# Kernel optimization log

Measured on AMD Instinct MI355X. Metric: run time of the kernel, lower is better.

The kernel has to match this reference:

```python
import jax, jax.numpy as jnp
import numpy as np

DIM = 2048
NUM_LADDERS = 3
DEPTH = 5
EPS = 0.01


def setup_inputs() -> dict:
    key = jax.random.key(0)
    ks = jax.random.split(key, 5)
    s = 1.0 / np.sqrt(DIM)
    x = jax.random.normal(ks[0], (4, 2048, DIM), dtype=jnp.float32)
    U_w = jax.random.uniform(ks[1], (DIM, DIM), jnp.float32, -s, s)          # U.weight  [out,in]
    gate_w = jax.random.uniform(ks[2], (DIM, DIM), jnp.float32, -s, s)       # gate_proj.weight
    ladder_w = jax.random.uniform(ks[3], (NUM_LADDERS, DEPTH + 1, DIM), jnp.float32, -s, s)
    V_w = jax.random.uniform(ks[4], (DIM, NUM_LADDERS), jnp.float32, -1.0 / np.sqrt(NUM_LADDERS), 1.0 / np.sqrt(NUM_LADDERS))
    return {"x": x, "U_w": U_w, "gate_w": gate_w, "ladder_w": ladder_w, "V_w": V_w}


def _continued_fraction(a_cf, eps):
    # a_cf: (..., depth). Evaluate a_1/(1 + a_2/(1 + ... a_d/1)) with
    # epsilon-guarded denominators (pole avoidance).
    d = a_cf.shape[-1]
    f = jnp.zeros(a_cf.shape[:-1], a_cf.dtype)
    for k in reversed(range(d)):  # tiny fixed depth: loop is fine
        denom = 1.0 + f
        denom = jnp.where(jnp.abs(denom) < eps,
                          jnp.where(denom >= 0, eps, -eps), denom)
        f = a_cf[..., k] / denom
    return f


def reference(x, U_w, gate_w, ladder_w, V_w):
    linear_out = jnp.einsum('bsd,od->bso', x, U_w)                 # U(x)
    gated_x = jax.nn.sigmoid(jnp.einsum('bsd,od->bso', x, gate_w)) * x
    # All ladders at once: (b,s,L,depth+1)
    a = jnp.einsum('bsd,lkd->bslk', gated_x, ladder_w)
    a0 = a[..., 0]                                                 # (b,s,L)
    z = a0 + _continued_fraction(a[..., 1:], EPS)                  # (b,s,L)
    combined = jnp.einsum('bsl,dl->bsd', z, V_w)                   # V(z)
    return linear_out + combined
```

## Files before the change

### kernel.cpp

```cpp
#include <hip/hip_runtime.h>
#include <cstdint>
#include <cstddef>

#define DIM 2048
#define NROWS 8192
#define NL 3
#define DEPTH 5
#define CF_EPS 0.01f

typedef __attribute__((ext_vector_type(8))) __bf16 bfrag;
typedef __attribute__((ext_vector_type(4))) float f32x4;

typedef __attribute__((address_space(1))) void gvoid;
typedef __attribute__((address_space(3))) void lvoid;

__device__ __forceinline__ void gld_lds16(const void* g, void* l) {
    __builtin_amdgcn_global_load_lds((gvoid*)g, (lvoid*)l, 16, 0, 0);
}

template<bool SPLIT>
__global__ __launch_bounds__(256) void mfma_gemm(
    const ushort* __restrict__ Ah, const ushort* __restrict__ Al,
    const ushort* __restrict__ Bh, const ushort* __restrict__ Bl,
    float* __restrict__ C)
{
    constexpr int BK = 32;
    __shared__ __align__(16) ushort sAh[128 * BK];
    __shared__ __align__(16) ushort sBh[128 * BK];
    __shared__ __align__(16) ushort sAl[SPLIT ? 128 * BK : 8];
    __shared__ __align__(16) ushort sBl[SPLIT ? 128 * BK : 8];

    const int tid  = threadIdx.x;
    const int wave = tid >> 6;
    const int lane = tid & 63;
    const int wm   = wave & 1;
    const int wn   = wave >> 1;
    const int m0   = blockIdx.y * 128;
    const int n0   = blockIdx.x * 128;

    const size_t soff = (size_t)(wave * 32 + (lane >> 2)) * DIM + (lane & 3) * 8;
    const ushort* gA  = Ah + (size_t)m0 * DIM + soff;
    const ushort* gB  = Bh + (size_t)n0 * DIM + soff;
    const ushort* gAl = Al + (size_t)m0 * DIM + soff;
    const ushort* gBl = Bl + (size_t)n0 * DIM + soff;

    ushort* lA0 = &sAh[(wave * 32) * BK];
    ushort* lA1 = &sAh[(wave * 32 + 16) * BK];
    ushort* lB0 = &sBh[(wave * 32) * BK];
    ushort* lB1 = &sBh[(wave * 32 + 16) * BK];
    ushort* lAl0 = &sAl[SPLIT ? (wave * 32) * BK : 0];
    ushort* lAl1 = &sAl[SPLIT ? (wave * 32 + 16) * BK : 0];
    ushort* lBl0 = &sBl[SPLIT ? (wave * 32) * BK : 0];
    ushort* lBl1 = &sBl[SPLIT ? (wave * 32 + 16) * BK : 0];

    const int fm = lane & 15;
    const int fq = lane >> 4;

    f32x4 acc[4][4];
    #pragma unroll
    for (int i = 0; i < 4; ++i)
        #pragma unroll
        for (int j = 0; j < 4; ++j)
            acc[i][j] = (f32x4){0.f, 0.f, 0.f, 0.f};

    for (int k0 = 0; k0 < DIM; k0 += BK) {
        __syncthreads();
        gld_lds16(gA + k0, lA0);
        gld_lds16(gA + (size_t)16 * DIM + k0, lA1);
        gld_lds16(gB + k0, lB0);
        gld_lds16(gB + (size_t)16 * DIM + k0, lB1);
        if constexpr (SPLIT) {
            gld_lds16(gAl + k0, lAl0);
            gld_lds16(gAl + (size_t)16 * DIM + k0, lAl1);
            gld_lds16(gBl + k0, lBl0);
            gld_lds16(gBl + (size_t)16 * DIM + k0, lBl1);
        }
        __syncthreads();

        bfrag ah[4], bh[4], al[4], bl[4];
        #pragma unroll
        for (int i = 0; i < 4; ++i) {
            ah[i] = *(const bfrag*)&sAh[(wm * 64 + i * 16 + fm) * BK + fq * 8];
            bh[i] = *(const bfrag*)&sBh[(wn * 64 + i * 16 + fm) * BK + fq * 8];
            if constexpr (SPLIT) {
                al[i] = *(const bfrag*)&sAl[(wm * 64 + i * 16 + fm) * BK + fq * 8];
                bl[i] = *(const bfrag*)&sBl[(wn * 64 + i * 16 + fm) * BK + fq * 8];
            }
        }
        #pragma unroll
        for (int i = 0; i < 4; ++i)
            #pragma unroll
            for (int j = 0; j < 4; ++j) {
                acc[i][j] = __builtin_amdgcn_mfma_f32_16x16x32_bf16(ah[i], bh[j], acc[i][j], 0, 0, 0);
                if constexpr (SPLIT) {
                    acc[i][j] = __builtin_amdgcn_mfma_f32_16x16x32_bf16(ah[i], bl[j], acc[i][j], 0, 0, 0);
                    acc[i][j] = __builtin_amdgcn_mfma_f32_16x16x32_bf16(al[i], bh[j], acc[i][j], 0, 0, 0);
                }
            }
    }

    #pragma unroll
    for (int i = 0; i < 4; ++i) {
        const int rowb = m0 + wm * 64 + i * 16 + fq * 4;
        #pragma unroll
        for (int j = 0; j < 4; ++j) {
            const int col = n0 + wn * 64 + j * 16 + fm;
            #pragma unroll
            for (int r = 0; r < 4; ++r)
                C[(size_t)(rowb + r) * DIM + col] = acc[i][j][r];
        }
    }
}

__device__ __forceinline__ ushort f2bf_bits(float f) {
    __bf16 h = (__bf16)f;
    return __builtin_bit_cast(unsigned short, h);
}
__device__ __forceinline__ float bfbits2f(ushort u) {
    __bf16 h = __builtin_bit_cast(__bf16, u);
    return (float)h;
}

union U16x8 { ushort u[8]; uint4 v; };

__global__ __launch_bounds__(256) void split2(const float* __restrict__ src,
                                              ushort* __restrict__ hi,
                                              ushort* __restrict__ lo)
{
    const size_t i0 = ((size_t)blockIdx.x * 256 + threadIdx.x) * 8;
    const float4 v0 = *(const float4*)(src + i0);
    const float4 v1 = *(const float4*)(src + i0 + 4);
    const float f[8] = {v0.x, v0.y, v0.z, v0.w, v1.x, v1.y, v1.z, v1.w};
    U16x8 h, l;
    #pragma unroll
    for (int j = 0; j < 8; ++j) {
        const ushort hb = f2bf_bits(f[j]);
        h.u[j] = hb;
        l.u[j] = f2bf_bits(f[j] - bfbits2f(hb));
    }
    *(uint4*)(hi + i0) = h.v;
    *(uint4*)(lo + i0) = l.v;
}

__global__ __launch_bounds__(256) void tobf16(const float* __restrict__ src,
                                              ushort* __restrict__ dst)
{
    const size_t i0 = ((size_t)blockIdx.x * 256 + threadIdx.x) * 8;
    const float4 v0 = *(const float4*)(src + i0);
    const float4 v1 = *(const float4*)(src + i0 + 4);
    const float f[8] = {v0.x, v0.y, v0.z, v0.w, v1.x, v1.y, v1.z, v1.w};
    U16x8 h;
    #pragma unroll
    for (int j = 0; j < 8; ++j) h.u[j] = f2bf_bits(f[j]);
    *(uint4*)(dst + i0) = h.v;
}

#define BMF 128
#define BNF 128
#define BKF 16
#define LDAF 132

__global__ __launch_bounds__(256) void sgemm_dual(
    const float* __restrict__ X,
    const float* __restrict__ Uw,
    const float* __restrict__ Gw,
    float* __restrict__ outLin,
    float* __restrict__ outGate)
{
    __shared__ float As[BKF][LDAF];
    __shared__ float Bs[BKF][LDAF];

    const int tid = threadIdx.x;
    const int n0 = blockIdx.x * BNF;
    const int m0 = blockIdx.y * BMF;
    const bool isGate = (n0 >= DIM);
    const float* W = isGate ? Gw : Uw;
    float* C = isGate ? outGate : outLin;
    const int nb = isGate ? (n0 - DIM) : n0;

    const int lr = tid >> 2;
    const int lc = (tid & 3) << 2;

    const float* pa0 = X + (size_t)(m0 + lr) * DIM + lc;
    const float* pa1 = X + (size_t)(m0 + lr + 64) * DIM + lc;
    const float* pb0 = W + (size_t)(nb + lr) * DIM + lc;
    const float* pb1 = W + (size_t)(nb + lr + 64) * DIM + lc;

    const int tx = tid & 15;
    const int ty = tid >> 4;

    float acc[8][8];
    #pragma unroll
    for (int i = 0; i < 8; ++i)
        #pragma unroll
        for (int j = 0; j < 8; ++j) acc[i][j] = 0.f;

    for (int k0 = 0; k0 < DIM; k0 += BKF) {
        const float4 a0 = *(const float4*)(pa0 + k0);
        const float4 a1 = *(const float4*)(pa1 + k0);
        const float4 b0 = *(const float4*)(pb0 + k0);
        const float4 b1 = *(const float4*)(pb1 + k0);
        __syncthreads();
        As[lc + 0][lr] = a0.x; As[lc + 1][lr] = a0.y; As[lc + 2][lr] = a0.z; As[lc + 3][lr] = a0.w;
        As[lc + 0][lr + 64] = a1.x; As[lc + 1][lr + 64] = a1.y; As[lc + 2][lr + 64] = a1.z; As[lc + 3][lr + 64] = a1.w;
        Bs[lc + 0][lr] = b0.x; Bs[lc + 1][lr] = b0.y; Bs[lc + 2][lr] = b0.z; Bs[lc + 3][lr] = b0.w;
        Bs[lc + 0][lr + 64] = b1.x; Bs[lc + 1][lr + 64] = b1.y; Bs[lc + 2][lr + 64] = b1.z; Bs[lc + 3][lr + 64] = b1.w;
        __syncthreads();
        #pragma unroll
        for (int kk = 0; kk < BKF; ++kk) {
            float av[8], bv[8];
            *(float4*)&av[0] = *(const float4*)&As[kk][ty * 8];
            *(float4*)&av[4] = *(const float4*)&As[kk][ty * 8 + 4];
            *(float4*)&bv[0] = *(const float4*)&Bs[kk][tx * 8];
            *(float4*)&bv[4] = *(const float4*)&Bs[kk][tx * 8 + 4];
            #pragma unroll
            for (int i = 0; i < 8; ++i)
                #pragma unroll
                for (int j = 0; j < 8; ++j)
                    acc[i][j] = fmaf(av[i], bv[j], acc[i][j]);
        }
    }

    #pragma unroll
    for (int i = 0; i < 8; ++i) {
        float* crow = C + (size_t)(m0 + ty * 8 + i) * DIM + nb + tx * 8;
        *(float4*)crow       = make_float4(acc[i][0], acc[i][1], acc[i][2], acc[i][3]);
        *(float4*)(crow + 4) = make_float4(acc[i][4], acc[i][5], acc[i][6], acc[i][7]);
    }
}

__global__ __launch_bounds__(256) void ladder_epilogue(
    const float* __restrict__ X,
    const float* __restrict__ G,
    const float* __restrict__ Lw,
    const float* __restrict__ Vw,
    float* __restrict__ Out)
{
    const int r = blockIdx.x;
    const int tid = threadIdx.x;
    const int d0 = tid * 8;
    const float* xrow = X + (size_t)r * DIM;
    const float* grow = G + (size_t)r * DIM;

    const float4 xv0 = *(const float4*)(xrow + d0);
    const float4 xv1 = *(const float4*)(xrow + d0 + 4);
    const float4 gv0 = *(const float4*)(grow + d0);
    const float4 gv1 = *(const float4*)(grow + d0 + 4);

    float gated[8];
    {
        const float gx[8] = {gv0.x, gv0.y, gv0.z, gv0.w, gv1.x, gv1.y, gv1.z, gv1.w};
        const float xx[8] = {xv0.x, xv0.y, xv0.z, xv0.w, xv1.x, xv1.y, xv1.z, xv1.w};
        #pragma unroll
        for (int j = 0; j < 8; ++j) {
            const float s = 1.0f / (1.0f + __expf(-gx[j]));
            gated[j] = s * xx[j];
        }
    }

    float part[NL * (DEPTH + 1)];
    #pragma unroll
    for (int lk = 0; lk < NL * (DEPTH + 1); ++lk) {
        const float* lrow = Lw + (size_t)lk * DIM + d0;
        const float4 w0 = *(const float4*)lrow;
        const float4 w1 = *(const float4*)(lrow + 4);
        part[lk] = gated[0] * w0.x + gated[1] * w0.y + gated[2] * w0.z + gated[3] * w0.w
                 + gated[4] * w1.x + gated[5] * w1.y + gated[6] * w1.z + gated[7] * w1.w;
    }

    #pragma unroll
    for (int off = 32; off > 0; off >>= 1) {
        #pragma unroll
        for (int lk = 0; lk < NL * (DEPTH + 1); ++lk)
            part[lk] += __shfl_down(part[lk], off, 64);
    }

    __shared__ float red[4][NL * (DEPTH + 1)];
    __shared__ float zsh[NL];
    const int wave = tid >> 6;
    const int lane = tid & 63;
    if (lane == 0) {
        #pragma unroll
        for (int lk = 0; lk < NL * (DEPTH + 1); ++lk) red[wave][lk] = part[lk];
    }
    __syncthreads();
    if (tid < NL) {
        float a[DEPTH + 1];
        #pragma unroll
        for (int k = 0; k < DEPTH + 1; ++k)
            a[k] = red[0][tid * 6 + k] + red[1][tid * 6 + k]
                 + red[2][tid * 6 + k] + red[3][tid * 6 + k];
        float f = 0.f;
        #pragma unroll
        for (int k = DEPTH - 1; k >= 0; --k) {
            float denom = 1.f + f;
            if (fabsf(denom) < CF_EPS) denom = (denom >= 0.f) ? CF_EPS : -CF_EPS;
            f = a[k + 1] / denom;
        }
        zsh[tid] = a[0] + f;
    }
    __syncthreads();
    const float z0 = zsh[0], z1 = zsh[1], z2 = zsh[2];

    float* orow = Out + (size_t)r * DIM + d0;
    const float4 o0 = *(const float4*)orow;
    const float4 o1 = *(const float4*)(orow + 4);
    float ov[8] = {o0.x, o0.y, o0.z, o0.w, o1.x, o1.y, o1.z, o1.w};
    #pragma unroll
    for (int j = 0; j < 8; ++j) {
        const float* vp = Vw + (size_t)(d0 + j) * NL;
        ov[j] += z0 * vp[0] + z1 * vp[1] + z2 * vp[2];
    }
    *(float4*)orow       = make_float4(ov[0], ov[1], ov[2], ov[3]);
    *(float4*)(orow + 4) = make_float4(ov[4], ov[5], ov[6], ov[7]);
}

extern "C" void kernel_launch(void* const* d_in, const int* in_sizes, int n_in,
                              void* d_out, int out_size, void* d_ws, size_t ws_size,
                              hipStream_t stream) {
    const float* X  = (const float*)d_in[0];
    const float* Uw = (const float*)d_in[1];
    const float* Gw = (const float*)d_in[2];
    const float* Lw = (const float*)d_in[3];
    const float* Vw = (const float*)d_in[4];
    float* out = (float*)d_out;

    const size_t WS_NEED = 159383552ull;
    char* ws = (char*)d_ws;
    float* gbuf = (float*)ws;

    if (ws_size >= WS_NEED) {
        ushort* Xh  = (ushort*)(ws + 67108864);
        ushort* Xl  = (ushort*)(ws + 100663296);
        ushort* Gwh = (ushort*)(ws + 134217728);
        ushort* Gwl = (ushort*)(ws + 142606336);
        ushort* Uwh = (ushort*)(ws + 150994944);

        split2<<<dim3(8192), dim3(256), 0, stream>>>(X, Xh, Xl);
        split2<<<dim3(2048), dim3(256), 0, stream>>>(Gw, Gwh, Gwl);
        tobf16<<<dim3(2048), dim3(256), 0, stream>>>(Uw, Uwh);

        dim3 grid(DIM / 128, NROWS / 128);
        mfma_gemm<false><<<grid, dim3(256), 0, stream>>>(Xh, Xh, Uwh, Uwh, out);
        mfma_gemm<true ><<<grid, dim3(256), 0, stream>>>(Xh, Xl, Gwh, Gwl, gbuf);
    } else {
        dim3 grid(2 * DIM / BNF, NROWS / BMF);
        sgemm_dual<<<grid, dim3(256), 0, stream>>>(X, Uw, Gw, out, gbuf);
    }
    ladder_epilogue<<<dim3(NROWS), dim3(256), 0, stream>>>(X, gbuf, Lw, Vw, out);
}
```

Measured before the change: 577.9 us.

## Fuse ladder projection into gate GEMM epilogue and V(z) into U GEMM

```diff
diff --git a/kernel.cpp b/kernel.cpp
--- a/kernel.cpp
+++ b/kernel.cpp
@@ -6,6 +6,7 @@
 #define NROWS 8192
 #define NL 3
 #define DEPTH 5
+#define NLK 18
 #define CF_EPS 0.01f
 
 typedef __attribute__((ext_vector_type(8))) __bf16 bfrag;
@@ -18,17 +19,14 @@
     __builtin_amdgcn_global_load_lds((gvoid*)g, (lvoid*)l, 16, 0, 0);
 }
 
-template<bool SPLIT>
-__global__ __launch_bounds__(256) void mfma_gemm(
-    const ushort* __restrict__ Ah, const ushort* __restrict__ Al,
-    const ushort* __restrict__ Bh, const ushort* __restrict__ Bl,
+__global__ __launch_bounds__(256) void mfma_gemm_u(
+    const ushort* __restrict__ A, const ushort* __restrict__ B,
+    const float* __restrict__ zb, const float* __restrict__ Vp,
     float* __restrict__ C)
 {
     constexpr int BK = 32;
-    __shared__ __align__(16) ushort sAh[128 * BK];
-    __shared__ __align__(16) ushort sBh[128 * BK];
-    __shared__ __align__(16) ushort sAl[SPLIT ? 128 * BK : 8];
-    __shared__ __align__(16) ushort sBl[SPLIT ? 128 * BK : 8];
+    __shared__ __align__(16) ushort sA[128 * BK];
+    __shared__ __align__(16) ushort sB[128 * BK];
 
     const int tid  = threadIdx.x;
     const int wave = tid >> 6;
@@ -39,19 +37,13 @@
     const int n0   = blockIdx.x * 128;
 
     const size_t soff = (size_t)(wave * 32 + (lane >> 2)) * DIM + (lane & 3) * 8;
-    const ushort* gA  = Ah + (size_t)m0 * DIM + soff;
-    const ushort* gB  = Bh + (size_t)n0 * DIM + soff;
-    const ushort* gAl = Al + (size_t)m0 * DIM + soff;
-    const ushort* gBl = Bl + (size_t)n0 * DIM + soff;
-
-    ushort* lA0 = &sAh[(wave * 32) * BK];
-    ushort* lA1 = &sAh[(wave * 32 + 16) * BK];
-    ushort* lB0 = &sBh[(wave * 32) * BK];
-    ushort* lB1 = &sBh[(wave * 32 + 16) * BK];
-    ushort* lAl0 = &sAl[SPLIT ? (wave * 32) * BK : 0];
-    ushort* lAl1 = &sAl[SPLIT ? (wave * 32 + 16) * BK : 0];
-    ushort* lBl0 = &sBl[SPLIT ? (wave * 32) * BK : 0];
-    ushort* lBl1 = &sBl[SPLIT ? (wave * 32 + 16) * BK : 0];
+    const ushort* gA = A + (size_t)m0 * DIM + soff;
+    const ushort* gB = B + (size_t)n0 * DIM + soff;
+
+    ushort* lA0 = &sA[(wave * 32) * BK];
+    ushort* lA1 = &sA[(wave * 32 + 16) * BK];
+    ushort* lB0 = &sB[(wave * 32) * BK];
+    ushort* lB1 = &sB[(wave * 32 + 16) * BK];
 
     const int fm = lane & 15;
     const int fq = lane >> 4;
@@ -69,12 +61,100 @@
         gld_lds16(gA + (size_t)16 * DIM + k0, lA1);
         gld_lds16(gB + k0, lB0);
         gld_lds16(gB + (size_t)16 * DIM + k0, lB1);
-        if constexpr (SPLIT) {
-            gld_lds16(gAl + k0, lAl0);
-            gld_lds16(gAl + (size_t)16 * DIM + k0, lAl1);
-            gld_lds16(gBl + k0, lBl0);
-            gld_lds16(gBl + (size_t)16 * DIM + k0, lBl1);
-        }
+        __syncthreads();
+
+        bfrag ah[4], bh[4];
+        #pragma unroll
+        for (int i = 0; i < 4; ++i) {
+            ah[i] = *(const bfrag*)&sA[(wm * 64 + i * 16 + fm) * BK + fq * 8];
+            bh[i] = *(const bfrag*)&sB[(wn * 64 + i * 16 + fm) * BK + fq * 8];
+        }
+        #pragma unroll
+        for (int i = 0; i < 4; ++i)
+            #pragma unroll
+            for (int j = 0; j < 4; ++j)
+                acc[i][j] = __builtin_amdgcn_mfma_f32_16x16x32_bf16(ah[i], bh[j], acc[i][j], 0, 0, 0);
+    }
+
+    float4 vc[4];
+    #pragma unroll
+    for (int j = 0; j < 4; ++j)
+        vc[j] = *(const float4*)&Vp[(size_t)(n0 + wn * 64 + j * 16 + fm) * 4];
+
+    #pragma unroll
+    for (int i = 0; i < 4; ++i) {
+        const int rowb = m0 + wm * 64 + i * 16 + fq * 4;
+        #pragma unroll
+        for (int r = 0; r < 4; ++r) {
+            const float4 zr = *(const float4*)&zb[(size_t)(rowb + r) * 4];
+            #pragma unroll
+            for (int j = 0; j < 4; ++j) {
+                const int col = n0 + wn * 64 + j * 16 + fm;
+                C[(size_t)(rowb + r) * DIM + col] =
+                    acc[i][j][r] + zr.x * vc[j].x + zr.y * vc[j].y + zr.z * vc[j].z;
+            }
+        }
+    }
+}
+
+__global__ __launch_bounds__(256) void mfma_gemm_gate(
+    const ushort* __restrict__ Ah, const ushort* __restrict__ Al,
+    const ushort* __restrict__ Bh, const ushort* __restrict__ Bl,
+    const float* __restrict__ X,  const float* __restrict__ Lw,
+    float* __restrict__ a_buf)
+{
+    constexpr int BK = 32;
+    __shared__ __align__(16) char smem[32768];
+    ushort* sAh = (ushort*)(smem);
+    ushort* sBh = (ushort*)(smem + 8192);
+    ushort* sAl = (ushort*)(smem + 16384);
+    ushort* sBl = (ushort*)(smem + 24576);
+    float*  sG  = (float*)(smem);
+    float*  sLw = (float*)(smem + 16896);
+
+    const int tid  = threadIdx.x;
+    const int wave = tid >> 6;
+    const int lane = tid & 63;
+    const int wm   = wave & 1;
+    const int wn   = wave >> 1;
+    const int m0   = blockIdx.y * 128;
+    const int n0   = blockIdx.x * 128;
+
+    const size_t soff = (size_t)(wave * 32 + (lane >> 2)) * DIM + (lane & 3) * 8;
+    const ushort* gA  = Ah + (size_t)m0 * DIM + soff;
+    const ushort* gAl = Al + (size_t)m0 * DIM + soff;
+    const ushort* gB  = Bh + (size_t)n0 * DIM + soff;
+    const ushort* gBl = Bl + (size_t)n0 * DIM + soff;
+
+    ushort* lA0  = &sAh[(wave * 32) * BK];
+    ushort* lA1  = &sAh[(wave * 32 + 16) * BK];
+    ushort* lB0  = &sBh[(wave * 32) * BK];
+    ushort* lB1  = &sBh[(wave * 32 + 16) * BK];
+    ushort* lAl0 = &sAl[(wave * 32) * BK];
+    ushort* lAl1 = &sAl[(wave * 32 + 16) * BK];
+    ushort* lBl0 = &sBl[(wave * 32) * BK];
+    ushort* lBl1 = &sBl[(wave * 32 + 16) * BK];
+
+    const int fm = lane & 15;
+    const int fq = lane >> 4;
+
+    f32x4 acc[4][4];
+    #pragma unroll
+    for (int i = 0; i < 4; ++i)
+        #pragma unroll
+        for (int j = 0; j < 4; ++j)
+            acc[i][j] = (f32x4){0.f, 0.f, 0.f, 0.f};
+
+    for (int k0 = 0; k0 < DIM; k0 += BK) {
+        __syncthreads();
+        gld_lds16(gA + k0, lA0);
+        gld_lds16(gA + (size_t)16 * DIM + k0, lA1);
+        gld_lds16(gB + k0, lB0);
+        gld_lds16(gB + (size_t)16 * DIM + k0, lB1);
+        gld_lds16(gAl + k0, lAl0);
+        gld_lds16(gAl + (size_t)16 * DIM + k0, lAl1);
+        gld_lds16(gBl + k0, lBl0);
+        gld_lds16(gBl + (size_t)16 * DIM + k0, lBl1);
         __syncthreads();
 
         bfrag ah[4], bh[4], al[4], bl[4];
@@ -82,34 +162,108 @@
         for (int i = 0; i < 4; ++i) {
             ah[i] = *(const bfrag*)&sAh[(wm * 64 + i * 16 + fm) * BK + fq * 8];
             bh[i] = *(const bfrag*)&sBh[(wn * 64 + i * 16 + fm) * BK + fq * 8];
-            if constexpr (SPLIT) {
-                al[i] = *(const bfrag*)&sAl[(wm * 64 + i * 16 + fm) * BK + fq * 8];
-                bl[i] = *(const bfrag*)&sBl[(wn * 64 + i * 16 + fm) * BK + fq * 8];
-            }
+            al[i] = *(const bfrag*)&sAl[(wm * 64 + i * 16 + fm) * BK + fq * 8];
+            bl[i] = *(const bfrag*)&sBl[(wn * 64 + i * 16 + fm) * BK + fq * 8];
         }
         #pragma unroll
         for (int i = 0; i < 4; ++i)
             #pragma unroll
             for (int j = 0; j < 4; ++j) {
                 acc[i][j] = __builtin_amdgcn_mfma_f32_16x16x32_bf16(ah[i], bh[j], acc[i][j], 0, 0, 0);
-                if constexpr (SPLIT) {
-                    acc[i][j] = __builtin_amdgcn_mfma_f32_16x16x32_bf16(ah[i], bl[j], acc[i][j], 0, 0, 0);
-                    acc[i][j] = __builtin_amdgcn_mfma_f32_16x16x32_bf16(al[i], bh[j], acc[i][j], 0, 0, 0);
+                acc[i][j] = __builtin_amdgcn_mfma_f32_16x16x32_bf16(ah[i], bl[j], acc[i][j], 0, 0, 0);
+                acc[i][j] = __builtin_amdgcn_mfma_f32_16x16x32_bf16(al[i], bh[j], acc[i][j], 0, 0, 0);
+            }
+    }
+
+    const float* xblk = X + (size_t)m0 * DIM + n0;
+    const int rred  = ((tid >> 6) << 3) | (tid & 7);
+    const int strip = (lane >> 3) & 7;
+    const int qc    = strip * 16;
+
+    for (int q = 0; q < 4; ++q) {
+        __syncthreads();
+        if (q == 0) {
+            for (int idx = tid; idx < NLK * 128; idx += 256) {
+                const int lk = idx >> 7, c = idx & 127;
+                sLw[lk * 156 + c + ((c >> 4) << 2)] = Lw[(size_t)lk * DIM + n0 + c];
+            }
+        }
+        if (wm == (q >> 1)) {
+            const int ib = (q & 1) * 2;
+            #pragma unroll
+            for (int ii = 0; ii < 2; ++ii) {
+                #pragma unroll
+                for (int r = 0; r < 4; ++r) {
+                    const int rloc = ii * 16 + fq * 4 + r;
+                    const float* xr = xblk + (size_t)(q * 32 + rloc) * DIM;
+                    #pragma unroll
+                    for (int j = 0; j < 4; ++j) {
+                        const int cc = wn * 64 + j * 16 + fm;
+                        const float g = acc[ib + ii][j][r];
+                        const float s = 1.0f / (1.0f + __expf(-g));
+                        sG[rloc * 132 + cc] = s * xr[cc];
+                    }
                 }
             }
-    }
-
-    #pragma unroll
-    for (int i = 0; i < 4; ++i) {
-        const int rowb = m0 + wm * 64 + i * 16 + fq * 4;
-        #pragma unroll
-        for (int j = 0; j < 4; ++j) {
-            const int col = n0 + wn * 64 + j * 16 + fm;
-            #pragma unroll
-            for (int r = 0; r < 4; ++r)
-                C[(size_t)(rowb + r) * DIM + col] = acc[i][j][r];
-        }
-    }
+        }
+        __syncthreads();
+
+        float p[NLK];
+        #pragma unroll
+        for (int lk = 0; lk < NLK; ++lk) p[lk] = 0.f;
+        #pragma unroll
+        for (int c4 = 0; c4 < 16; c4 += 4) {
+            const float4 g4 = *(const float4*)&sG[rred * 132 + qc + c4];
+            #pragma unroll
+            for (int lk = 0; lk < NLK; ++lk) {
+                const float4 w4 = *(const float4*)&sLw[lk * 156 + qc + c4 + (strip << 2)];
+                p[lk] = fmaf(g4.x, w4.x, fmaf(g4.y, w4.y,
+                        fmaf(g4.z, w4.z, fmaf(g4.w, w4.w, p[lk]))));
+            }
+        }
+        #pragma unroll
+        for (int lk = 0; lk < NLK; ++lk) {
+            p[lk] += __shfl_xor(p[lk], 8, 64);
+            p[lk] += __shfl_xor(p[lk], 16, 64);
+            p[lk] += __shfl_xor(p[lk], 32, 64);
+        }
+        if ((lane >> 3) == 0) {
+            float* dst = a_buf + (size_t)(m0 + q * 32 + rred) * NLK;
+            #pragma unroll
+            for (int lk = 0; lk < NLK; ++lk) atomicAdd(dst + lk, p[lk]);
+        }
+    }
+}
+
+__global__ __launch_bounds__(256) void cf_kernel(const float* __restrict__ a_buf,
+                                                 float* __restrict__ zb)
+{
+    const int r = blockIdx.x * 256 + threadIdx.x;
+    const float* ar = a_buf + (size_t)r * NLK;
+    float z[NL];
+    #pragma unroll
+    for (int l = 0; l < NL; ++l) {
+        float a[DEPTH + 1];
+        #pragma unroll
+        for (int k = 0; k <= DEPTH; ++k) a[k] = ar[l * (DEPTH + 1) + k];
+        float f = 0.f;
+        #pragma unroll
+        for (int k = DEPTH - 1; k >= 0; --k) {
+            float denom = 1.f + f;
+            if (fabsf(denom) < CF_EPS) denom = (denom >= 0.f) ? CF_EPS : -CF_EPS;
+            f = a[k + 1] / denom;
+        }
+        z[l] = a[0] + f;
+    }
+    *(float4*)&zb[(size_t)r * 4] = make_float4(z[0], z[1], z[2], 0.f);
+}
+
+__global__ __launch_bounds__(256) void padV(const float* __restrict__ Vw,
+                                            float* __restrict__ Vp)
+{
+    const int d = blockIdx.x * 256 + threadIdx.x;
+    *(float4*)&Vp[(size_t)d * 4] =
+        make_float4(Vw[(size_t)d * 3], Vw[(size_t)d * 3 + 1], Vw[(size_t)d * 3 + 2], 0.f);
 }
 
 __device__ __forceinline__ ushort f2bf_bits(float f) {
@@ -258,9 +412,9 @@
         }
     }
 
-    float part[NL * (DEPTH + 1)];
-    #pragma unroll
-    for (int lk = 0; lk < NL * (DEPTH + 1); ++lk) {
+    float part[NLK];
+    #pragma unroll
+    for (int lk = 0; lk < NLK; ++lk) {
         const float* lrow = Lw + (size_t)lk * DIM + d0;
         const float4 w0 = *(const float4*)lrow;
         const float4 w1 = *(const float4*)(lrow + 4);
@@ -271,17 +425,17 @@
     #pragma unroll
     for (int off = 32; off > 0; off >>= 1) {
         #pragma unroll
-        for (int lk = 0; lk < NL * (DEPTH + 1); ++lk)
+        for (int lk = 0; lk < NLK; ++lk)
             part[lk] += __shfl_down(part[lk], off, 64);
     }
 
-    __shared__ float red[4][NL * (DEPTH + 1)];
+    __shared__ float red[4][NLK];
     __shared__ float zsh[NL];
     const int wave = tid >> 6;
     const int lane = tid & 63;
     if (lane == 0) {
         #pragma unroll
-        for (int lk = 0; lk < NL * (DEPTH + 1); ++lk) red[wave][lk] = part[lk];
+        for (int lk = 0; lk < NLK; ++lk) red[wave][lk] = part[lk];
     }
     __syncthreads();
     if (tid < NL) {
@@ -325,27 +479,33 @@
     const float* Vw = (const float*)d_in[4];
     float* out = (float*)d_out;
 
-    const size_t WS_NEED = 159383552ull;
+    const size_t WS_NEED = 93028352ull;
     char* ws = (char*)d_ws;
-    float* gbuf = (float*)ws;
 
     if (ws_size >= WS_NEED) {
-        ushort* Xh  = (ushort*)(ws + 67108864);
-        ushort* Xl  = (ushort*)(ws + 100663296);
-        ushort* Gwh = (ushort*)(ws + 134217728);
-        ushort* Gwl = (ushort*)(ws + 142606336);
-        ushort* Uwh = (ushort*)(ws + 150994944);
+        ushort* Xh    = (ushort*)(ws);
+        ushort* Xl    = (ushort*)(ws + 33554432);
+        ushort* Gwh   = (ushort*)(ws + 67108864);
+        ushort* Gwl   = (ushort*)(ws + 75497472);
+        ushort* Uwh   = (ushort*)(ws + 83886080);
+        float*  a_buf = (float*)(ws + 92274688);
+        float*  z_buf = (float*)(ws + 92864512);
+        float*  Vp    = (float*)(ws + 92995584);
 
         split2<<<dim3(8192), dim3(256), 0, stream>>>(X, Xh, Xl);
         split2<<<dim3(2048), dim3(256), 0, stream>>>(Gw, Gwh, Gwl);
         tobf16<<<dim3(2048), dim3(256), 0, stream>>>(Uw, Uwh);
+        padV  <<<dim3(8),    dim3(256), 0, stream>>>(Vw, Vp);
+        hipMemsetAsync(a_buf, 0, (size_t)NROWS * NLK * sizeof(float), stream);
 
         dim3 grid(DIM / 128, NROWS / 128);
-        mfma_gemm<false><<<grid, dim3(256), 0, stream>>>(Xh, Xh, Uwh, Uwh, out);
-        mfma_gemm<true ><<<grid, dim3(256), 0, stream>>>(Xh, Xl, Gwh, Gwl, gbuf);
+        mfma_gemm_gate<<<grid, dim3(256), 0, stream>>>(Xh, Xl, Gwh, Gwl, X, Lw, a_buf);
+        cf_kernel<<<dim3(32), dim3(256), 0, stream>>>(a_buf, z_buf);
+        mfma_gemm_u<<<grid, dim3(256), 0, stream>>>(Xh, Uwh, z_buf, Vp, out);
     } else {
+        float* gbuf = (float*)ws;
         dim3 grid(2 * DIM / BNF, NROWS / BMF);
         sgemm_dual<<<grid, dim3(256), 0, stream>>>(X, Uw, Gw, out, gbuf);
-    }
-    ladder_epilogue<<<dim3(NROWS), dim3(256), 0, stream>>>(X, gbuf, Lw, Vw, out);
-}
+        ladder_epilogue<<<dim3(NROWS), dim3(256), 0, stream>>>(X, gbuf, Lw, Vw, out);
+    }
+}
```

New measurement: 1.199 ms. +107.5%, slower.
